# Performance work log

Hardware: AMD Instinct MI355X
Metric: run time of the kernel (lower is better)

The kernel has to match this reference:

```python
import jax, jax.numpy as jnp
import numpy as np

N_NODES = 50000
N_REL = 4
N_EDGES = 800000
IN_DIM = 128
HID = 128
N_CLASSES = 16


def setup_inputs() -> dict:
    key = jax.random.key(0)
    ks = jax.random.split(key, 12)
    feat = jax.random.normal(ks[0], (N_NODES, IN_DIM), dtype=jnp.float32)
    src = jax.random.randint(ks[1], (N_REL, N_EDGES), 0, N_NODES, dtype=jnp.int32)
    dst = jax.random.randint(ks[2], (N_REL, N_EDGES), 0, N_NODES, dtype=jnp.int32)
    s = 0.05
    W1 = jax.random.normal(ks[3], (N_REL, IN_DIM, HID), dtype=jnp.float32) * s
    b1 = jax.random.normal(ks[4], (N_REL, HID), dtype=jnp.float32) * s
    W2 = jax.random.normal(ks[5], (N_REL, HID, HID), dtype=jnp.float32) * s
    b2 = jax.random.normal(ks[6], (N_REL, HID), dtype=jnp.float32) * s
    W3 = jax.random.normal(ks[7], (N_REL, HID, HID), dtype=jnp.float32) * s
    b3 = jax.random.normal(ks[8], (N_REL, HID), dtype=jnp.float32) * s
    Wlin = jax.random.normal(ks[9], (HID, N_CLASSES), dtype=jnp.float32) * s
    blin = jax.random.normal(ks[10], (N_CLASSES,), dtype=jnp.float32) * s
    return {"feat": feat, "src": src, "dst": dst, "W1": W1, "b1": b1,
            "W2": W2, "b2": b2, "W3": W3, "b3": b3, "Wlin": Wlin, "blin": blin}


def _graph_conv(x, s, d, W, b, n_nodes):
    """DGL GraphConv with norm='both': D_dst^-1/2 * A * D_src^-1/2 * x, then @W + b."""
    ones = jnp.ones(s.shape[0], dtype=x.dtype)
    deg_out = jnp.maximum(jax.ops.segment_sum(ones, s, num_segments=n_nodes), 1.0)
    deg_in = jnp.maximum(jax.ops.segment_sum(ones, d, num_segments=n_nodes), 1.0)
    xs = x * (deg_out ** -0.5)[:, None]          # [N, F]
    agg = jax.ops.segment_sum(xs[s], d, num_segments=n_nodes)  # gather+scatter [N, F]
    agg = agg * (deg_in ** -0.5)[:, None]
    return agg @ W + b


def _hetero_layer(x, src, dst, W, b, n_nodes):
    # HeteroGraphConv aggregate='sum' over relations (loop over small fixed R)
    out = _graph_conv(x, src[0], dst[0], W[0], b[0], n_nodes)
    for r in range(1, src.shape[0]):
        out = out + _graph_conv(x, src[r], dst[r], W[r], b[r], n_nodes)
    return out


def _l2_normalize(x, eps=1e-12):
    # torch F.normalize: x / max(||x||_2, eps), per row
    nrm = jnp.sqrt(jnp.sum(x * x, axis=1, keepdims=True))
    return x / jnp.maximum(nrm, eps)


def reference(feat, src, dst, W1, b1, W2, b2, W3, b3, Wlin, blin):
    n = feat.shape[0]
    h = _hetero_layer(feat, src, dst, W1, b1, n)
    h = jax.nn.leaky_relu(_l2_normalize(h), negative_slope=0.01)
    h = _hetero_layer(h, src, dst, W2, b2, n)
    h = jax.nn.leaky_relu(_l2_normalize(h), negative_slope=0.01)
    h = _hetero_layer(h, src, dst, W3, b3, n)
    # update_all(copy_u, sum) across all relations (unnormalized scatter-sum)
    pooled = jax.ops.segment_sum(h[src[0]], dst[0], num_segments=n)
    for r in range(1, src.shape[0]):
        pooled = pooled + jax.ops.segment_sum(h[src[r]], dst[r], num_segments=n)
    hg = jnp.mean(pooled, axis=0, keepdims=True)  # dgl.mean_nodes -> [1, HID]
    return jax.nn.sigmoid(hg @ Wlin + blin)       # [1, n_classes]
```

## Files before the change

### kernel.cpp

```cpp
#include <hip/hip_runtime.h>
#include <hip/hip_bf16.h>

constexpr int N_NODES = 50000;
constexpr int N_REL   = 4;
constexpr int N_EDGES = 800000;
constexpr int DIM     = 128;
constexpr int N_CLS   = 16;

constexpr int CHUNK  = 256;
constexpr int NCHUNK = (N_NODES + CHUNK - 1) / CHUNK;
constexpr int NPART  = N_REL * NCHUNK;

constexpr int NCBR  = (N_NODES + 255) / 256;
constexpr int NCB   = N_REL * NCBR;
constexpr int TILE  = 8000;
constexpr int TPR   = N_EDGES / TILE;
constexpr int MAXB  = 6144;

constexpr int RNG    = 12544;
constexpr int NRANGE = 4;
constexpr int DTILE  = 80000;
constexpr int DNT    = N_EDGES / DTILE;

constexpr int NPB = 8;
constexpr int CAP = 512;

constexpr int N_PAD = 50048;

constexpr float YSCALE = 32.0f;

typedef __attribute__((ext_vector_type(8))) short short8;
typedef __attribute__((ext_vector_type(4))) float float4v;
typedef __attribute__((ext_vector_type(2))) float floatx2;

__device__ __forceinline__ unsigned int f2bf_bits(float f) {
  unsigned int u = __float_as_uint(f);
  return (u + 0x7fffu + ((u >> 16) & 1u)) >> 16;
}
__device__ __forceinline__ unsigned int pack2bf(float a, float b) {
  return f2bf_bits(a) | (f2bf_bits(b) << 16);
}
__device__ __forceinline__ float bf_lo(unsigned int u) { return __uint_as_float(u << 16); }
__device__ __forceinline__ float bf_hi(unsigned int u) { return __uint_as_float(u & 0xffff0000u); }

__device__ __forceinline__ int LCOL(int p) { return (p & 7) * 16 + (p >> 3); }

__global__ __launch_bounds__(256) void degree_hist(
    const int* __restrict__ src, const int* __restrict__ dst,
    int* __restrict__ cnt_out, int* __restrict__ cnt_in) {
  int b = blockIdx.x;
  int t     = b % DNT;    b /= DNT;
  int range = b % NRANGE; b /= NRANGE;
  int r     = b % N_REL;  b /= N_REL;
  int which = b;
  const int* arr = (which ? dst : src) + (size_t)r * N_EDGES + (size_t)t * DTILE;
  int* cnt = (which ? cnt_in : cnt_out) + r * N_NODES;
  int tid = threadIdx.x;
  __shared__ int h[RNG];
  for (int i = tid; i < RNG; i += 256) h[i] = 0;
  __syncthreads();
  int lo = range * RNG;
  int hi = lo + RNG;
  const int4* a4 = (const int4*)arr;
  for (int i = tid; i < DTILE / 4; i += 256) {
    int4 v = a4[i];
    if (v.x >= lo && v.x < hi) atomicAdd(&h[v.x - lo], 1);
    if (v.y >= lo && v.y < hi) atomicAdd(&h[v.y - lo], 1);
    if (v.z >= lo && v.z < hi) atomicAdd(&h[v.z - lo], 1);
    if (v.w >= lo && v.w < hi) atomicAdd(&h[v.w - lo], 1);
  }
  __syncthreads();
  for (int i = tid; i < RNG; i += 256) {
    int n = lo + i;
    int c = h[i];
    if (n < N_NODES && c) atomicAdd(&cnt[n], c);
  }
}

__global__ __launch_bounds__(256) void scan_partial(
    const int* __restrict__ cnt_in, int* __restrict__ partial) {
  int b = blockIdx.x;
  int r = b / NCHUNK, c = b % NCHUNK;
  int i = c * CHUNK + threadIdx.x;
  int v = (i < N_NODES) ? cnt_in[r * N_NODES + i] : 0;
#pragma unroll
  for (int off = 1; off < 64; off <<= 1) v += __shfl_xor(v, off, 64);
  __shared__ int ws[4];
  if ((threadIdx.x & 63) == 0) ws[threadIdx.x >> 6] = v;
  __syncthreads();
  if (threadIdx.x == 0) partial[b] = ws[0] + ws[1] + ws[2] + ws[3];
}

__global__ __launch_bounds__(1024) void scan_offsets(
    const int* __restrict__ partial, int* __restrict__ chunk_off,
    int* __restrict__ row_ptr) {
  __shared__ int lds[1024];
  __shared__ int sexcl[1024];
  __shared__ int stotal;
  int tid = threadIdx.x;
  int v = (tid < NPART) ? partial[tid] : 0;
  lds[tid] = v;
  __syncthreads();
  for (int off = 1; off < 1024; off <<= 1) {
    int t = (tid >= off) ? lds[tid - off] : 0;
    __syncthreads();
    lds[tid] += t;
    __syncthreads();
  }
  int excl = lds[tid] - v;
  sexcl[tid] = excl;
  if (tid == NPART - 1) stotal = excl + v;
  if (tid < NPART) chunk_off[tid] = excl;
  __syncthreads();
  if (tid < N_REL) {
    int base = sexcl[tid * NCHUNK];
    int next = (tid < N_REL - 1) ? sexcl[(tid + 1) * NCHUNK] : stotal;
    row_ptr[tid * (N_NODES + 1) + N_NODES] = next - base;
  }
}

__global__ __launch_bounds__(256) void scan_expand(
    const int* __restrict__ cnt_in, const int* __restrict__ chunk_off,
    int* __restrict__ row_ptr, int* __restrict__ cbcur,
    const int* __restrict__ cnt_out, float* __restrict__ soutF,
    float* __restrict__ sinF, float* __restrict__ wout) {
  int b = blockIdx.x;
  int r = b / NCHUNK, c = b % NCHUNK;
  int tid = threadIdx.x;
  int i = c * CHUNK + tid;
  int v = (i < N_NODES) ? cnt_in[r * N_NODES + i] : 0;
  __shared__ int lds[CHUNK];
  lds[tid] = v;
  __syncthreads();
  for (int off = 1; off < CHUNK; off <<= 1) {
    int t = (tid >= off) ? lds[tid - off] : 0;
    __syncthreads();
    lds[tid] += t;
    __syncthreads();
  }
  int excl = lds[tid] - v;
  int base = chunk_off[b] - chunk_off[r * NCHUNK];
  if (i < N_NODES) {
    row_ptr[r * (N_NODES + 1) + i] = base + excl;
    int co = cnt_out[r * N_NODES + i];
    soutF[r * N_NODES + i] = YSCALE / sqrtf((float)max(co, 1));
    sinF [r * N_NODES + i] = (1.0f / YSCALE) / sqrtf((float)max(v, 1));
    if (r == 0) {
      wout[i] = (float)(co + cnt_out[N_NODES + i] +
                        cnt_out[2 * N_NODES + i] + cnt_out[3 * N_NODES + i]);
    }
  }
  if (tid == 0) cbcur[r * NCBR + c] = base;
}

__global__ __launch_bounds__(256) void pass1_bin(
    const int* __restrict__ src, const int* __restrict__ dst,
    int* __restrict__ cbcur, unsigned int* __restrict__ binned) {
  int b = blockIdx.x;
  int r = b / TPR, t = b % TPR;
  const int* sp = src + (size_t)r * N_EDGES + t * TILE;
  const int* dp = dst + (size_t)r * N_EDGES + t * TILE;
  unsigned int* outp = binned + (size_t)r * N_EDGES;
  int tid = threadIdx.x;
  __shared__ int hist[NCBR];
  __shared__ int scanb[256];
  __shared__ int gbase[NCBR];
  __shared__ int lcur[NCBR];
  for (int i = tid; i < NCBR; i += 256) hist[i] = 0;
  __syncthreads();
  for (int i = tid; i < TILE; i += 256) atomicAdd(&hist[dp[i] >> 8], 1);
  __syncthreads();
  int v = (tid < NCBR) ? hist[tid] : 0;
  scanb[tid] = v;
  __syncthreads();
  for (int off = 1; off < 256; off <<= 1) {
    int tv = (tid >= off) ? scanb[tid - off] : 0;
    __syncthreads();
    scanb[tid] += tv;
    __syncthreads();
  }
  if (tid < NCBR) {
    int excl = scanb[tid] - v;
    gbase[tid] = atomicAdd(&cbcur[r * NCBR + tid], v) - excl;
    lcur[tid] = excl;
  }
  __syncthreads();
  for (int i = tid; i < TILE; i += 256) {
    int d = dp[i];
    int s = sp[i];
    int cb = d >> 8;
    int lp = atomicAdd(&lcur[cb], 1);
    outp[gbase[cb] + lp] = ((unsigned)s << 8) | (unsigned)(d & 255);
  }
}

__global__ __launch_bounds__(256) void pass2_sort(
    const unsigned int* __restrict__ binned, const int* __restrict__ row_ptr,
    unsigned short* __restrict__ csr) {
  int b = blockIdx.x;
  int r = b / NCBR, c = b % NCBR;
  int node0 = c * 256;
  int node1 = min(node0 + 256, N_NODES);
  int start = row_ptr[r * (N_NODES + 1) + node0];
  int endv  = row_ptr[r * (N_NODES + 1) + node1];
  int count = endv - start;
  const unsigned int* bp = binned + (size_t)r * N_EDGES + start;
  unsigned short* outg = csr + (size_t)r * N_EDGES + start;
  int tid = threadIdx.x;
  __shared__ int hist[256];
  __shared__ int scanb[256];
  __shared__ unsigned short outb[MAXB];
  hist[tid] = 0;
  __syncthreads();
  for (int i = tid; i < count; i += 256) atomicAdd(&hist[bp[i] & 255u], 1);
  __syncthreads();
  int v = hist[tid];
  scanb[tid] = v;
  __syncthreads();
  for (int off = 1; off < 256; off <<= 1) {
    int tv = (tid >= off) ? scanb[tid - off] : 0;
    __syncthreads();
    scanb[tid] += tv;
    __syncthreads();
  }
  hist[tid] = scanb[tid] - v;
  __syncthreads();
  if (count <= MAXB) {
    for (int i = tid; i < count; i += 256) {
      unsigned int p = bp[i];
      int pos = atomicAdd(&hist[p & 255u], 1);
      outb[pos] = (unsigned short)(p >> 8);
    }
    __syncthreads();
    for (int i = tid; i < count; i += 256) outg[i] = outb[i];
  } else {
    for (int i = tid; i < count; i += 256) {
      unsigned int p = bp[i];
      int pos = atomicAdd(&hist[p & 255u], 1);
      outg[pos] = (unsigned short)(p >> 8);
    }
  }
}

__global__ __launch_bounds__(256) void prep_w3(
    const float* __restrict__ W1, const float* __restrict__ b1,
    const float* __restrict__ W2, const float* __restrict__ b2,
    const float* __restrict__ W3, const float* __restrict__ b3,
    unsigned short* __restrict__ Wt1, float* __restrict__ bs1,
    unsigned short* __restrict__ Wt2, float* __restrict__ bs2,
    unsigned short* __restrict__ Wt3, float* __restrict__ bs3) {
  int set = blockIdx.x >> 8;
  int i   = (blockIdx.x & 255) * 256 + threadIdx.x;
  const float* W = (set == 0) ? W1 : (set == 1) ? W2 : W3;
  const float* b = (set == 0) ? b1 : (set == 1) ? b2 : b3;
  unsigned short* Wt = (set == 0) ? Wt1 : (set == 1) ? Wt2 : Wt3;
  float* bsum = (set == 0) ? bs1 : (set == 1) ? bs2 : bs3;
  int permk = (set != 0);
  if (i < N_REL * DIM * DIM) {
    int col = i >> 7, p = i & 127;
    int k = permk ? LCOL(p) : p;
    int rrel = col >> 7, n = col & 127;
    Wt[i] = (unsigned short)f2bf_bits(W[rrel * DIM * DIM + k * DIM + n]);
  }
  if (i < DIM) {
    int Lp = LCOL(i);
    bsum[i] = b[Lp] + b[DIM + Lp] + b[2 * DIM + Lp] + b[3 * DIM + Lp];
  }
}

__global__ __launch_bounds__(256) void zero_pad(unsigned char* __restrict__ Yb) {
  constexpr int PER = (N_PAD - N_NODES) * DIM / 16;
  int tid = blockIdx.x * 256 + threadIdx.x;
  int r = tid / PER, k = tid % PER;
  if (r < N_REL) {
    uint4* p = (uint4*)(Yb + (size_t)r * N_PAD * DIM + (size_t)N_NODES * DIM);
    p[k] = make_uint4(0u, 0u, 0u, 0u);
  }
}

template <int AF32>
__global__ __launch_bounds__(256) void gemm_y(
    const void* __restrict__ Xv, const unsigned short* __restrict__ Wt,
    const float* __restrict__ soutF, unsigned char* __restrict__ Yb) {
  int tid = threadIdx.x;
  int w   = tid >> 6;
  int l   = tid & 63;
  int l15 = l & 15, lq = l >> 4;
  int rowbase = blockIdx.x * 64;

  const unsigned short* X = (const unsigned short*)Xv;
  const float*          Xf = (const float*)Xv;

  float4v acc[4][8] = {};
  const unsigned short* Wq = Wt + (size_t)(w * DIM) * DIM;

#pragma unroll
  for (int ks = 0; ks < 4; ++ks) {
    int k0 = ks * 32 + lq * 8;
    short8 bfr[8];
#pragma unroll
    for (int c = 0; c < 8; ++c)
      bfr[c] = *(const short8*)(Wq + (size_t)(c * 16 + l15) * DIM + k0);
#pragma unroll
    for (int i = 0; i < 4; ++i) {
      int rr = rowbase + i * 16 + l15;
      short8 afr;
      if (rr < N_NODES) {
        if (AF32) {
          const float* xp = Xf + (size_t)rr * DIM + k0;
          float4 f0 = *(const float4*)xp;
          float4 f1 = *(const float4*)(xp + 4);
          afr[0] = (short)f2bf_bits(f0.x);
          afr[1] = (short)f2bf_bits(f0.y);
          afr[2] = (short)f2bf_bits(f0.z);
          afr[3] = (short)f2bf_bits(f0.w);
          afr[4] = (short)f2bf_bits(f1.x);
          afr[5] = (short)f2bf_bits(f1.y);
          afr[6] = (short)f2bf_bits(f1.z);
          afr[7] = (short)f2bf_bits(f1.w);
        } else {
          afr = *(const short8*)(X + (size_t)rr * DIM + k0);
        }
      } else {
        afr = (short8)(short)0;
      }
#pragma unroll
      for (int c = 0; c < 8; ++c)
        acc[i][c] = __builtin_amdgcn_mfma_f32_16x16x32_bf16(afr, bfr[c],
                                                            acc[i][c], 0, 0, 0);
    }
  }

  const float* so = soutF + (size_t)w * N_NODES;
  unsigned char* Yq = Yb + (size_t)w * N_PAD * DIM;
#pragma unroll
  for (int i = 0; i < 4; ++i) {
#pragma unroll
    for (int rr = 0; rr < 4; ++rr) {
      int grow = rowbase + i * 16 + lq * 4 + rr;
      if (grow < N_NODES) {
        float sc = so[grow];
        float v0 = acc[i][0][rr] * sc, v1 = acc[i][1][rr] * sc;
        float v2 = acc[i][2][rr] * sc, v3 = acc[i][3][rr] * sc;
        float v4 = acc[i][4][rr] * sc, v5 = acc[i][5][rr] * sc;
        float v6 = acc[i][6][rr] * sc, v7 = acc[i][7][rr] * sc;
        int t0 = __builtin_amdgcn_cvt_pk_fp8_f32(v0, v1, 0, false);
        t0 = __builtin_amdgcn_cvt_pk_fp8_f32(v2, v3, t0, true);
        int t1 = __builtin_amdgcn_cvt_pk_fp8_f32(v4, v5, 0, false);
        t1 = __builtin_amdgcn_cvt_pk_fp8_f32(v6, v7, t1, true);
        uint2 o;
        o.x = (unsigned)t0;
        o.y = (unsigned)t1;
        *(uint2*)(Yq + (size_t)grow * DIM + l15 * 8) = o;
      }
    }
  }
}

template <int MODE>
__global__ __launch_bounds__(256) void gather_y(
    const unsigned char* __restrict__ Yb, const unsigned short* __restrict__ csr,
    const int* __restrict__ row_ptr, const float* __restrict__ sinF,
    const float* __restrict__ bsum, void* __restrict__ out) {
  int d0   = blockIdx.x * NPB;
  int r    = threadIdx.x >> 6;
  int lane = threadIdx.x & 63;
  int g    = lane >> 4;
  int l16  = lane & 15;
  const unsigned short* cs = csr + (size_t)r * N_EDGES;
  const unsigned char*  Yq = Yb + (size_t)r * N_PAD * DIM;

  int rp = row_ptr[r * (N_NODES + 1) + d0 + min(lane, NPB)];
  int beg0 = __shfl(rp, 0, 64);
  int cnt  = __shfl(rp, NPB, 64) - beg0;

  __shared__ unsigned short scsr[N_REL][CAP];
  __shared__ __align__(16) unsigned int ubuf[N_REL][NPB][66];

  int ccap = min(cnt, CAP);
  for (int i = lane; i < ccap; i += 64) scsr[r][i] = cs[beg0 + i];

  auto body = [&](auto CS) {
#pragma unroll 1
    for (int n = 0; n < NPB; n += 2) {
      int bA = __shfl(rp, n, 64),  eA = __shfl(rp, n + 1, 64);
      int bB = eA,                 eB = __shfl(rp, n + 2, 64);
      floatx2 aA[4], aB[4];
#pragma unroll
      for (int j = 0; j < 4; ++j) {
        aA[j] = (floatx2){0.f, 0.f};
        aB[j] = (floatx2){0.f, 0.f};
      }
      int pA = bA, pB = bB;
      while (pA < eA || pB < eB) {
        bool doA = pA < eA, doB = pB < eB;
        uint2 xA[4], xB[4];
        if (doA) {
#pragma unroll
          for (int u = 0; u < 4; ++u) {
            int e = pA + u * 4 + g;
            int se = (e < eA) ? (int)CS(e) : N_NODES;
            xA[u] = *(const uint2*)(Yq + (size_t)se * DIM + l16 * 8);
          }
        }
        if (doB) {
#pragma unroll
          for (int u = 0; u < 4; ++u) {
            int e = pB + u * 4 + g;
            int se = (e < eB) ? (int)CS(e) : N_NODES;
            xB[u] = *(const uint2*)(Yq + (size_t)se * DIM + l16 * 8);
          }
        }
        if (doA) {
#pragma unroll
          for (int u = 0; u < 4; ++u) {
            aA[0] += __builtin_amdgcn_cvt_pk_f32_fp8((int)xA[u].x, false);
            aA[1] += __builtin_amdgcn_cvt_pk_f32_fp8((int)xA[u].x, true);
            aA[2] += __builtin_amdgcn_cvt_pk_f32_fp8((int)xA[u].y, false);
            aA[3] += __builtin_amdgcn_cvt_pk_f32_fp8((int)xA[u].y, true);
          }
          pA += 16;
        }
        if (doB) {
#pragma unroll
          for (int u = 0; u < 4; ++u) {
            aB[0] += __builtin_amdgcn_cvt_pk_f32_fp8((int)xB[u].x, false);
            aB[1] += __builtin_amdgcn_cvt_pk_f32_fp8((int)xB[u].x, true);
            aB[2] += __builtin_amdgcn_cvt_pk_f32_fp8((int)xB[u].y, false);
            aB[3] += __builtin_amdgcn_cvt_pk_f32_fp8((int)xB[u].y, true);
          }
          pB += 16;
        }
      }
#pragma unroll
      for (int j = 0; j < 4; ++j) {
        aA[j].x += __shfl_xor(aA[j].x, 16, 64);
        aA[j].y += __shfl_xor(aA[j].y, 16, 64);
        aA[j].x += __shfl_xor(aA[j].x, 32, 64);
        aA[j].y += __shfl_xor(aA[j].y, 32, 64);
        aB[j].x += __shfl_xor(aB[j].x, 16, 64);
        aB[j].y += __shfl_xor(aB[j].y, 16, 64);
        aB[j].x += __shfl_xor(aB[j].x, 32, 64);
        aB[j].y += __shfl_xor(aB[j].y, 32, 64);
      }
      if (g < 2) {
        uint2 wA, wB;
        if (g == 0) {
          wA.x = pack2bf(aA[0].x, aA[0].y); wA.y = pack2bf(aA[1].x, aA[1].y);
          wB.x = pack2bf(aB[0].x, aB[0].y); wB.y = pack2bf(aB[1].x, aB[1].y);
        } else {
          wA.x = pack2bf(aA[2].x, aA[2].y); wA.y = pack2bf(aA[3].x, aA[3].y);
          wB.x = pack2bf(aB[2].x, aB[2].y); wB.y = pack2bf(aB[3].x, aB[3].y);
        }
        *(uint2*)&ubuf[r][n][l16 * 4 + g * 2]     = wA;
        *(uint2*)&ubuf[r][n + 1][l16 * 4 + g * 2] = wB;
      }
    }
  };
  if (cnt <= CAP)
    body([&](int e) { return scsr[r][e - beg0]; });
  else
    body([&](int e) { return cs[e]; });
  __syncthreads();

  int nn = threadIdx.x >> 5;
  int ln = threadIdx.x & 31;
  int d  = d0 + nn;
  float s0 = sinF[d];
  float s1 = sinF[N_NODES + d];
  float s2 = sinF[2 * N_NODES + d];
  float s3 = sinF[3 * N_NODES + d];
  uint2 u0 = *(const uint2*)&ubuf[0][nn][ln * 2];
  uint2 u1 = *(const uint2*)&ubuf[1][nn][ln * 2];
  uint2 u2 = *(const uint2*)&ubuf[2][nn][ln * 2];
  uint2 u3 = *(const uint2*)&ubuf[3][nn][ln * 2];
  float4 bs = *(const float4*)&bsum[ln * 4];
  float v0 = s0 * bf_lo(u0.x) + s1 * bf_lo(u1.x) + s2 * bf_lo(u2.x) +
             s3 * bf_lo(u3.x) + bs.x;
  float v1 = s0 * bf_hi(u0.x) + s1 * bf_hi(u1.x) + s2 * bf_hi(u2.x) +
             s3 * bf_hi(u3.x) + bs.y;
  float v2 = s0 * bf_lo(u0.y) + s1 * bf_lo(u1.y) + s2 * bf_lo(u2.y) +
             s3 * bf_lo(u3.y) + bs.z;
  float v3 = s0 * bf_hi(u0.y) + s1 * bf_hi(u1.y) + s2 * bf_hi(u2.y) +
             s3 * bf_hi(u3.y) + bs.w;
  if (MODE == 1) {
    float ss = v0 * v0 + v1 * v1 + v2 * v2 + v3 * v3;
    ss += __shfl_xor(ss, 1, 32);
    ss += __shfl_xor(ss, 2, 32);
    ss += __shfl_xor(ss, 4, 32);
    ss += __shfl_xor(ss, 8, 32);
    ss += __shfl_xor(ss, 16, 32);
    float sc = 1.0f / fmaxf(sqrtf(ss), 1e-12f);
    v0 *= sc; v1 *= sc; v2 *= sc; v3 *= sc;
    v0 = v0 > 0.f ? v0 : 0.01f * v0;
    v1 = v1 > 0.f ? v1 : 0.01f * v1;
    v2 = v2 > 0.f ? v2 : 0.01f * v2;
    v3 = v3 > 0.f ? v3 : 0.01f * v3;
    uint2 o;
    o.x = pack2bf(v0, v1);
    o.y = pack2bf(v2, v3);
    *(uint2*)((unsigned short*)out + (size_t)d * DIM + ln * 4) = o;
  } else {
    float4 o = make_float4(v0, v1, v2, v3);
    *(float4*)((float*)out + (size_t)d * DIM + ln * 4) = o;
  }
}

__global__ __launch_bounds__(256) void pool_kernel(
    const float* __restrict__ h, const float* __restrict__ wout,
    float* __restrict__ hg) {
  int gw   = blockIdx.x * 4 + (threadIdx.x >> 6);
  int lane = threadIdx.x & 63;
  int nw   = gridDim.x * 4;
  float ax = 0.0f, ay = 0.0f;
  for (int v = gw; v < N_NODES; v += nw) {
    float w = wout[v];
    float2 hv = *(const float2*)(h + (size_t)v * DIM + lane * 2);
    ax = fmaf(w, hv.x, ax);
    ay = fmaf(w, hv.y, ay);
  }
  atomicAdd(&hg[lane * 2],     ax);
  atomicAdd(&hg[lane * 2 + 1], ay);
}

__global__ void head_kernel(const float* __restrict__ hg,
                            const float* __restrict__ Wlin,
                            const float* __restrict__ blin,
                            float* __restrict__ out) {
  int j = threadIdx.x;
  if (j < N_CLS) {
    float s = blin[j];
    const float invN = 1.0f / (float)N_NODES;
#pragma unroll 16
    for (int k = 0; k < DIM; ++k) {
      int Lk = (k & 7) * 16 + (k >> 3);
      s = fmaf(hg[k] * invN, Wlin[Lk * N_CLS + j], s);
    }
    out[j] = 1.0f / (1.0f + expf(-s));
  }
}

__global__ void fail_kernel(float* out) {
  int i = threadIdx.x;
  if (i < N_CLS) out[i] = 1e30f;
}

extern "C" void kernel_launch(void* const* d_in, const int* in_sizes, int n_in,
                              void* d_out, int out_size, void* d_ws, size_t ws_size,
                              hipStream_t stream) {
  const float* feat = (const float*)d_in[0];
  const int*   src  = (const int*)  d_in[1];
  const int*   dst  = (const int*)  d_in[2];
  const float* W1   = (const float*)d_in[3];
  const float* b1   = (const float*)d_in[4];
  const float* W2   = (const float*)d_in[5];
  const float* b2   = (const float*)d_in[6];
  const float* W3   = (const float*)d_in[7];
  const float* b3   = (const float*)d_in[8];
  const float* Wlin = (const float*)d_in[9];
  const float* blin = (const float*)d_in[10];
  float* out = (float*)d_out;

  char* base = (char*)d_ws;
  size_t off = 0;
  auto alloc = [&](size_t bytes) -> void* {
    void* q = base + off;
    off = (off + bytes + 255) & ~(size_t)255;
    return q;
  };
  int*   cnt_out  = (int*)  alloc((size_t)N_REL * N_NODES * 4);
  int*   cnt_in   = (int*)  alloc((size_t)N_REL * N_NODES * 4);
  int*   row_ptr  = (int*)  alloc((size_t)N_REL * (N_NODES + 1) * 4);
  float* soutF    = (float*)alloc((size_t)N_REL * N_NODES * 4);
  float* sinF     = (float*)alloc((size_t)N_REL * N_NODES * 4);
  float* wout     = (float*)alloc((size_t)N_NODES * 4);
  float* hg       = (float*)alloc((size_t)DIM * 4);
  int*   partial  = (int*)  alloc((size_t)NPART * 4);
  int*   chunkoff = (int*)  alloc((size_t)NPART * 4);
  int*   cbcur    = (int*)  alloc((size_t)NCB * 4);
  unsigned int*   binned = (unsigned int*)  alloc((size_t)N_REL * N_EDGES * 4);
  unsigned short* csr    = (unsigned short*)alloc((size_t)N_REL * N_EDGES * 2);
  unsigned char*  Yb     = (unsigned char*) alloc((size_t)N_REL * N_PAD * DIM);
  unsigned short* X1     = (unsigned short*)alloc((size_t)N_NODES * DIM * 2);
  unsigned short* X2     = (unsigned short*)alloc((size_t)N_NODES * DIM * 2);
  float* H3       = (float*)alloc((size_t)N_NODES * DIM * 4);
  unsigned short* Wt1 = (unsigned short*)alloc((size_t)N_REL * DIM * DIM * 2);
  unsigned short* Wt2 = (unsigned short*)alloc((size_t)N_REL * DIM * DIM * 2);
  unsigned short* Wt3 = (unsigned short*)alloc((size_t)N_REL * DIM * DIM * 2);
  float* bs1 = (float*)alloc(DIM * 4);
  float* bs2 = (float*)alloc(DIM * 4);
  float* bs3 = (float*)alloc(DIM * 4);

  if (off > ws_size) {
    fail_kernel<<<1, 64, 0, stream>>>(out);
    return;
  }

  hipMemsetAsync(cnt_out, 0, (size_t)2 * N_REL * N_NODES * 4, stream);
  hipMemsetAsync(hg, 0, DIM * 4, stream);

  degree_hist  <<<2 * N_REL * NRANGE * DNT, 256, 0, stream>>>(src, dst, cnt_out, cnt_in);
  scan_partial <<<NPART, 256, 0, stream>>>(cnt_in, partial);
  scan_offsets <<<1, 1024, 0, stream>>>(partial, chunkoff, row_ptr);
  scan_expand  <<<NPART, 256, 0, stream>>>(cnt_in, chunkoff, row_ptr, cbcur,
                                           cnt_out, soutF, sinF, wout);
  pass1_bin    <<<N_REL * TPR, 256, 0, stream>>>(src, dst, cbcur, binned);
  pass2_sort   <<<NCB, 256, 0, stream>>>(binned, row_ptr, csr);

  prep_w3<<<3 * 256, 256, 0, stream>>>(W1, b1, W2, b2, W3, b3,
                                       Wt1, bs1, Wt2, bs2, Wt3, bs3);
  zero_pad<<<6, 256, 0, stream>>>(Yb);

  int gemm_blocks = N_PAD / 64;
  int gath_blocks = (N_NODES + NPB - 1) / NPB;

  gemm_y<1>  <<<gemm_blocks, 256, 0, stream>>>(feat, Wt1, soutF, Yb);
  gather_y<1><<<gath_blocks, 256, 0, stream>>>(Yb, csr, row_ptr, sinF, bs1, X1);
  gemm_y<0>  <<<gemm_blocks, 256, 0, stream>>>(X1, Wt2, soutF, Yb);
  gather_y<1><<<gath_blocks, 256, 0, stream>>>(Yb, csr, row_ptr, sinF, bs2, X2);
  gemm_y<0>  <<<gemm_blocks, 256, 0, stream>>>(X2, Wt3, soutF, Yb);
  gather_y<0><<<gath_blocks, 256, 0, stream>>>(Yb, csr, row_ptr, sinF, bs3, H3);

  pool_kernel<<<256, 256, 0, stream>>>(H3, wout, hg);
  head_kernel<<<1, 64, 0, stream>>>(hg, Wlin, blin, out);
}
```

Baseline: 486.8 us.

## Derive CSR row pointers from coarse bin counts inside the sort pass

Replaces the fine-grained in-degree histogram and its three-kernel scan chain with a coarse per-256-node bin count over dst and a single bin scan. The local histogram in pass2_sort now also produces row_ptr, the in/out degree normalisation scales and the pooling weights, so the separate scan_expand pass is gone. This cuts launches and global traffic over cnt_in, at the cost of a coarse pass that rereads dst and extra per-node writes in the sort kernel.

```diff
diff --git a/kernel.cpp b/kernel.cpp
--- a/kernel.cpp
+++ b/kernel.cpp
@@ -7,10 +7,6 @@
 constexpr int DIM     = 128;
 constexpr int N_CLS   = 16;
 
-constexpr int CHUNK  = 256;
-constexpr int NCHUNK = (N_NODES + CHUNK - 1) / CHUNK;
-constexpr int NPART  = N_REL * NCHUNK;
-
 constexpr int NCBR  = (N_NODES + 255) / 256;
 constexpr int NCB   = N_REL * NCBR;
 constexpr int TILE  = 8000;
@@ -45,16 +41,14 @@
 
 __device__ __forceinline__ int LCOL(int p) { return (p & 7) * 16 + (p >> 3); }
 
-__global__ __launch_bounds__(256) void degree_hist(
-    const int* __restrict__ src, const int* __restrict__ dst,
-    int* __restrict__ cnt_out, int* __restrict__ cnt_in) {
+__global__ __launch_bounds__(256) void degree_hist_src(
+    const int* __restrict__ src, int* __restrict__ cnt_out) {
   int b = blockIdx.x;
   int t     = b % DNT;    b /= DNT;
   int range = b % NRANGE; b /= NRANGE;
-  int r     = b % N_REL;  b /= N_REL;
-  int which = b;
-  const int* arr = (which ? dst : src) + (size_t)r * N_EDGES + (size_t)t * DTILE;
-  int* cnt = (which ? cnt_in : cnt_out) + r * N_NODES;
+  int r     = b;
+  const int* arr = src + (size_t)r * N_EDGES + (size_t)t * DTILE;
+  int* cnt = cnt_out + r * N_NODES;
   int tid = threadIdx.x;
   __shared__ int h[RNG];
   for (int i = tid; i < RNG; i += 256) h[i] = 0;
@@ -77,28 +71,29 @@
   }
 }
 
-__global__ __launch_bounds__(256) void scan_partial(
-    const int* __restrict__ cnt_in, int* __restrict__ partial) {
+__global__ __launch_bounds__(256) void pass0_coarse(
+    const int* __restrict__ dst, int* __restrict__ binCnt) {
   int b = blockIdx.x;
-  int r = b / NCHUNK, c = b % NCHUNK;
-  int i = c * CHUNK + threadIdx.x;
-  int v = (i < N_NODES) ? cnt_in[r * N_NODES + i] : 0;
-#pragma unroll
-  for (int off = 1; off < 64; off <<= 1) v += __shfl_xor(v, off, 64);
-  __shared__ int ws[4];
-  if ((threadIdx.x & 63) == 0) ws[threadIdx.x >> 6] = v;
-  __syncthreads();
-  if (threadIdx.x == 0) partial[b] = ws[0] + ws[1] + ws[2] + ws[3];
-}
-
-__global__ __launch_bounds__(1024) void scan_offsets(
-    const int* __restrict__ partial, int* __restrict__ chunk_off,
-    int* __restrict__ row_ptr) {
+  int r = b / TPR, t = b % TPR;
+  const int* dp = dst + (size_t)r * N_EDGES + t * TILE;
+  int tid = threadIdx.x;
+  __shared__ int hist[NCBR];
+  for (int i = tid; i < NCBR; i += 256) hist[i] = 0;
+  __syncthreads();
+  for (int i = tid; i < TILE; i += 256) atomicAdd(&hist[dp[i] >> 8], 1);
+  __syncthreads();
+  for (int i = tid; i < NCBR; i += 256) {
+    int c = hist[i];
+    if (c) atomicAdd(&binCnt[r * NCBR + i], c);
+  }
+}
+
+__global__ __launch_bounds__(1024) void scan_bins(
+    const int* __restrict__ binCnt, int* __restrict__ bstart,
+    int* __restrict__ cbcur, int* __restrict__ row_ptr) {
   __shared__ int lds[1024];
-  __shared__ int sexcl[1024];
-  __shared__ int stotal;
   int tid = threadIdx.x;
-  int v = (tid < NPART) ? partial[tid] : 0;
+  int v = (tid < NCB) ? binCnt[tid] : 0;
   lds[tid] = v;
   __syncthreads();
   for (int off = 1; off < 1024; off <<= 1) {
@@ -108,49 +103,13 @@
     __syncthreads();
   }
   int excl = lds[tid] - v;
-  sexcl[tid] = excl;
-  if (tid == NPART - 1) stotal = excl + v;
-  if (tid < NPART) chunk_off[tid] = excl;
-  __syncthreads();
-  if (tid < N_REL) {
-    int base = sexcl[tid * NCHUNK];
-    int next = (tid < N_REL - 1) ? sexcl[(tid + 1) * NCHUNK] : stotal;
-    row_ptr[tid * (N_NODES + 1) + N_NODES] = next - base;
-  }
-}
-
-__global__ __launch_bounds__(256) void scan_expand(
-    const int* __restrict__ cnt_in, const int* __restrict__ chunk_off,
-    int* __restrict__ row_ptr, int* __restrict__ cbcur,
-    const int* __restrict__ cnt_out, float* __restrict__ soutF,
-    float* __restrict__ sinF, float* __restrict__ wout) {
-  int b = blockIdx.x;
-  int r = b / NCHUNK, c = b % NCHUNK;
-  int tid = threadIdx.x;
-  int i = c * CHUNK + tid;
-  int v = (i < N_NODES) ? cnt_in[r * N_NODES + i] : 0;
-  __shared__ int lds[CHUNK];
-  lds[tid] = v;
-  __syncthreads();
-  for (int off = 1; off < CHUNK; off <<= 1) {
-    int t = (tid >= off) ? lds[tid - off] : 0;
-    __syncthreads();
-    lds[tid] += t;
-    __syncthreads();
-  }
-  int excl = lds[tid] - v;
-  int base = chunk_off[b] - chunk_off[r * NCHUNK];
-  if (i < N_NODES) {
-    row_ptr[r * (N_NODES + 1) + i] = base + excl;
-    int co = cnt_out[r * N_NODES + i];
-    soutF[r * N_NODES + i] = YSCALE / sqrtf((float)max(co, 1));
-    sinF [r * N_NODES + i] = (1.0f / YSCALE) / sqrtf((float)max(v, 1));
-    if (r == 0) {
-      wout[i] = (float)(co + cnt_out[N_NODES + i] +
-                        cnt_out[2 * N_NODES + i] + cnt_out[3 * N_NODES + i]);
-    }
-  }
-  if (tid == 0) cbcur[r * NCBR + c] = base;
+  if (tid < NCB) {
+    bstart[tid] = excl;
+    int r = tid / NCBR;
+    cbcur[tid] = excl - r * N_EDGES;
+  }
+  if (tid == NCB - 1) bstart[NCB] = excl + v;
+  if (tid < N_REL) row_ptr[tid * (N_NODES + 1) + N_NODES] = N_EDGES;
 }
 
 __global__ __launch_bounds__(256) void pass1_bin(
@@ -195,15 +154,15 @@
 }
 
 __global__ __launch_bounds__(256) void pass2_sort(
-    const unsigned int* __restrict__ binned, const int* __restrict__ row_ptr,
-    unsigned short* __restrict__ csr) {
+    const unsigned int* __restrict__ binned, const int* __restrict__ bstart,
+    const int* __restrict__ cnt_out, int* __restrict__ row_ptr,
+    float* __restrict__ soutF, float* __restrict__ sinF,
+    float* __restrict__ wout, unsigned short* __restrict__ csr) {
   int b = blockIdx.x;
   int r = b / NCBR, c = b % NCBR;
-  int node0 = c * 256;
-  int node1 = min(node0 + 256, N_NODES);
-  int start = row_ptr[r * (N_NODES + 1) + node0];
-  int endv  = row_ptr[r * (N_NODES + 1) + node1];
-  int count = endv - start;
+  int gstart = bstart[b];
+  int count  = bstart[b + 1] - gstart;
+  int start  = gstart - r * N_EDGES;
   const unsigned int* bp = binned + (size_t)r * N_EDGES + start;
   unsigned short* outg = csr + (size_t)r * N_EDGES + start;
   int tid = threadIdx.x;
@@ -223,7 +182,20 @@
     scanb[tid] += tv;
     __syncthreads();
   }
-  hist[tid] = scanb[tid] - v;
+  int excl = scanb[tid] - v;
+  int node = c * 256 + tid;
+  if (node < N_NODES) {
+    row_ptr[r * (N_NODES + 1) + node] = start + excl;
+    sinF[r * N_NODES + node] = (1.0f / YSCALE) / sqrtf((float)max(v, 1));
+    int co = cnt_out[r * N_NODES + node];
+    soutF[r * N_NODES + node] = YSCALE / sqrtf((float)max(co, 1));
+    if (r == 0) {
+      wout[node] = (float)(co + cnt_out[N_NODES + node] +
+                           cnt_out[2 * N_NODES + node] +
+                           cnt_out[3 * N_NODES + node]);
+    }
+  }
+  hist[tid] = excl;
   __syncthreads();
   if (count <= MAXB) {
     for (int i = tid; i < count; i += 256) {
@@ -569,14 +541,13 @@
     return q;
   };
   int*   cnt_out  = (int*)  alloc((size_t)N_REL * N_NODES * 4);
-  int*   cnt_in   = (int*)  alloc((size_t)N_REL * N_NODES * 4);
   int*   row_ptr  = (int*)  alloc((size_t)N_REL * (N_NODES + 1) * 4);
   float* soutF    = (float*)alloc((size_t)N_REL * N_NODES * 4);
   float* sinF     = (float*)alloc((size_t)N_REL * N_NODES * 4);
   float* wout     = (float*)alloc((size_t)N_NODES * 4);
   float* hg       = (float*)alloc((size_t)DIM * 4);
-  int*   partial  = (int*)  alloc((size_t)NPART * 4);
-  int*   chunkoff = (int*)  alloc((size_t)NPART * 4);
+  int*   binCnt   = (int*)  alloc((size_t)NCB * 4);
+  int*   bstart   = (int*)  alloc((size_t)(NCB + 1) * 4);
   int*   cbcur    = (int*)  alloc((size_t)NCB * 4);
   unsigned int*   binned = (unsigned int*)  alloc((size_t)N_REL * N_EDGES * 4);
   unsigned short* csr    = (unsigned short*)alloc((size_t)N_REL * N_EDGES * 2);
@@ -596,16 +567,16 @@
     return;
   }
 
-  hipMemsetAsync(cnt_out, 0, (size_t)2 * N_REL * N_NODES * 4, stream);
+  hipMemsetAsync(cnt_out, 0, (size_t)N_REL * N_NODES * 4, stream);
+  hipMemsetAsync(binCnt, 0, (size_t)NCB * 4, stream);
   hipMemsetAsync(hg, 0, DIM * 4, stream);
 
-  degree_hist  <<<2 * N_REL * NRANGE * DNT, 256, 0, stream>>>(src, dst, cnt_out, cnt_in);
-  scan_partial <<<NPART, 256, 0, stream>>>(cnt_in, partial);
-  scan_offsets <<<1, 1024, 0, stream>>>(partial, chunkoff, row_ptr);
-  scan_expand  <<<NPART, 256, 0, stream>>>(cnt_in, chunkoff, row_ptr, cbcur,
-                                           cnt_out, soutF, sinF, wout);
-  pass1_bin    <<<N_REL * TPR, 256, 0, stream>>>(src, dst, cbcur, binned);
-  pass2_sort   <<<NCB, 256, 0, stream>>>(binned, row_ptr, csr);
+  degree_hist_src<<<N_REL * NRANGE * DNT, 256, 0, stream>>>(src, cnt_out);
+  pass0_coarse   <<<N_REL * TPR, 256, 0, stream>>>(dst, binCnt);
+  scan_bins      <<<1, 1024, 0, stream>>>(binCnt, bstart, cbcur, row_ptr);
+  pass1_bin      <<<N_REL * TPR, 256, 0, stream>>>(src, dst, cbcur, binned);
+  pass2_sort     <<<NCB, 256, 0, stream>>>(binned, bstart, cnt_out, row_ptr,
+                                           soutF, sinF, wout, csr);
 
   prep_w3<<<3 * 256, 256, 0, stream>>>(W1, b1, W2, b2, W3, b3,
                                        Wt1, bs1, Wt2, bs2, Wt3, bs3);
```

Result: no change. 484.3 us (-0.5%).
